# Kernel tuning notes

Hardware: AMD Instinct MI355X
Metric: run time of the kernel (lower is better)

## Reference

```python
import jax, jax.numpy as jnp
import numpy as np

N_S, N_G, E = 4000, 50000, 250000   # sample nodes, gene nodes, edges per relation
D, H, C1, C3 = 128, 4, 32, 64       # input dim, heads, layer-1 per-head dim, layer-3 per-head dim
NEG_SLOPE = 0.2


def gatv2(x_src, x_dst, src, dst, ea, Wl, bl, Wr, br, We, att, bias, n_dst, concat):
    """PyG GATv2Conv (add_self_loops=False, edge_dim=1, eval mode)."""
    Hh, C = att.shape
    xl = (x_src @ Wl + bl).reshape(-1, Hh, C)          # [N_src, H, C]
    xr = (x_dst @ Wr + br).reshape(-1, Hh, C)          # [N_dst, H, C]
    ee = (ea @ We).reshape(-1, Hh, C)                  # [E, H, C]
    m = jax.nn.leaky_relu(xl[src] + xr[dst] + ee, NEG_SLOPE)   # [E, H, C]
    logits = jnp.einsum('ehc,hc->eh', m, att)          # [E, H]
    # segment softmax over incoming edges of each destination node
    lmax = jax.ops.segment_max(logits, dst, num_segments=n_dst)[dst]
    ex = jnp.exp(logits - lmax)
    denom = jax.ops.segment_sum(ex, dst, num_segments=n_dst)[dst]
    alpha = ex / denom                                 # [E, H]
    out = jax.ops.segment_sum(xl[src] * alpha[:, :, None], dst, num_segments=n_dst)  # [N_dst, H, C]
    out = out.reshape(n_dst, Hh * C) if concat else out.mean(axis=1)
    return out + bias


def setup_inputs() -> dict:
    key = jax.random.key(0)
    ks = jax.random.split(key, 40)
    p = lambda i, shape: jax.random.normal(ks[i], shape, dtype=jnp.float32) * 0.05
    HC1, HC3 = H * C1, H * C3
    inp = {
        'x_mrna': p(0, (N_S, D)),
        'x_gene': p(1, (N_G, D)),
        'sg_src': jax.random.randint(ks[2], (E,), 0, N_S),
        'sg_dst': jax.random.randint(ks[3], (E,), 0, N_G),
        'gs_src': jax.random.randint(ks[4], (E,), 0, N_G),
        'gs_dst': jax.random.randint(ks[5], (E,), 0, N_S),
        'ea_sg': p(6, (E, 1)),
        'ea_gs': p(7, (E, 1)),
        # layer-1 GATv2 params, relation mrna->gene
        'Wl1_sg': p(8, (D, HC1)), 'bl1_sg': p(9, (HC1,)),
        'Wr1_sg': p(10, (D, HC1)), 'br1_sg': p(11, (HC1,)),
        'We1_sg': p(12, (1, HC1)), 'att1_sg': p(13, (H, C1)), 'bo1_sg': p(14, (HC1,)),
        # layer-1 GATv2 params, relation gene->mrna
        'Wl1_gs': p(15, (D, HC1)), 'bl1_gs': p(16, (HC1,)),
        'Wr1_gs': p(17, (D, HC1)), 'br1_gs': p(18, (HC1,)),
        'We1_gs': p(19, (1, HC1)), 'att1_gs': p(20, (H, C1)), 'bo1_gs': p(21, (HC1,)),
        # layer-3 GATv2 params, relation gene->mrna (concat=False)
        'Wl3_gs': p(22, (HC1, HC3)), 'bl3_gs': p(23, (HC3,)),
        'Wr3_gs': p(24, (HC1, HC3)), 'br3_gs': p(25, (HC3,)),
        'We3_gs': p(26, (1, HC3)), 'att3_gs': p(27, (H, C3)), 'bo3_gs': p(28, (C3,)),
        # self-loop linears for omic ('mrna') nodes
        'Wsl1': p(29, (D, C1)), 'bsl1': p(30, (C1,)),
        'Wsl3': p(31, (HC1, C3)), 'bsl3': p(32, (C3,)),
    }
    return inp


def reference(x_mrna, x_gene, sg_src, sg_dst, gs_src, gs_dst, ea_sg, ea_gs,
              Wl1_sg, bl1_sg, Wr1_sg, br1_sg, We1_sg, att1_sg, bo1_sg,
              Wl1_gs, bl1_gs, Wr1_gs, br1_gs, We1_gs, att1_gs, bo1_gs,
              Wl3_gs, bl3_gs, Wr3_gs, br3_gs, We3_gs, att3_gs, bo3_gs,
              Wsl1, bsl1, Wsl3, bsl3):
    # ---- layer 1 (HeteroConv over both relations) ----
    x1_gene = gatv2(x_mrna, x_gene, sg_src, sg_dst, ea_sg,
                    Wl1_sg, bl1_sg, Wr1_sg, br1_sg, We1_sg, att1_sg, bo1_sg, N_G, True)
    x1_mrna = gatv2(x_gene, x_mrna, gs_src, gs_dst, ea_gs,
                    Wl1_gs, bl1_gs, Wr1_gs, br1_gs, We1_gs, att1_gs, bo1_gs, N_S, True)
    # self-loop linear on omic nodes, repeated across heads (repeat(1, heads))
    x1_mrna = x1_mrna + jnp.tile(x_mrna @ Wsl1 + bsl1, (1, H))
    x1_mrna = jax.nn.relu(x1_mrna)
    x1_gene = jax.nn.relu(x1_gene)
    # ---- three_layers=False: x2 = x1; layer 3 (concat=False, head mean) ----
    x3_mrna = gatv2(x1_gene, x1_mrna, gs_src, gs_dst, ea_gs,
                    Wl3_gs, bl3_gs, Wr3_gs, br3_gs, We3_gs, att3_gs, bo3_gs, N_S, False)
    x3_mrna = x3_mrna + (x1_mrna @ Wsl3 + bsl3)
    x3_mrna = jax.nn.relu(x3_mrna)
    # integrator=None, single omic view -> squeeze to [N_S, C3]
    return x3_mrna
```

## Files before the change

kernel.cpp:

```cpp
#include <hip/hip_runtime.h>
#include <cstdint>
#include <cstddef>

#define NS 4000
#define NG 50000
#define NE 250000
#define DIM 128
#define NDST_TOT (NG + NS)

typedef __bf16 bf16_t;
typedef bf16_t bf16x8 __attribute__((ext_vector_type(8)));
typedef bf16_t bf16x4 __attribute__((ext_vector_type(4)));
typedef bf16_t bf16x2 __attribute__((ext_vector_type(2)));
typedef float floatx4 __attribute__((ext_vector_type(4)));

#define HIST_B 977
#define WT_TOT 143360
struct HPArgs {
  const int* sgd; const int* gsd;
  int* cnt; unsigned short* rank_sg; unsigned short* rank_gs;
  const float* W[8]; bf16_t* Wt[8]; int N[8]; int e0[8];
  const float* xm; bf16_t* xbm;
  const float* xg; bf16_t* xbg;
};

__global__ __launch_bounds__(256) void histprep(HPArgs a) {
  if (blockIdx.x < HIST_B) {
    int e = blockIdx.x * 256 + threadIdx.x;
    if (e < NE) {
      a.rank_sg[e] = (unsigned short)atomicAdd(a.cnt + a.sgd[e], 1);
      a.rank_gs[e] = (unsigned short)atomicAdd(a.cnt + NG + a.gsd[e], 1);
    }
  } else {
    int u = (blockIdx.x - HIST_B) * 256 + threadIdx.x;
    if (u < WT_TOT) {
      int c = 0;
#pragma unroll
      for (int i = 1; i < 8; i++) if (u >= a.e0[i]) c = i;
      int idx = u - a.e0[c];
      int N = a.N[c];
      int k = idx / N, n = idx - k * N;
      a.Wt[c][n * 128 + k] = (bf16_t)a.W[c][idx];
    } else if (u < WT_TOT + 128000) {
      int j = (u - WT_TOT) * 4;
      float4 v = *reinterpret_cast<const float4*>(a.xm + j);
      bf16x4 b;
      b[0] = (bf16_t)v.x; b[1] = (bf16_t)v.y; b[2] = (bf16_t)v.z; b[3] = (bf16_t)v.w;
      *reinterpret_cast<bf16x4*>(a.xbm + j) = b;
    } else {
      int j = (u - WT_TOT - 128000) * 4;
      float4 v = *reinterpret_cast<const float4*>(a.xg + j);
      bf16x4 b;
      b[0] = (bf16_t)v.x; b[1] = (bf16_t)v.y; b[2] = (bf16_t)v.z; b[3] = (bf16_t)v.w;
      *reinterpret_cast<bf16x4*>(a.xbg + j) = b;
    }
  }
}

__global__ __launch_bounds__(1024) void scan1(const int* __restrict__ cnt,
                                              int* __restrict__ rp,
                                              int* __restrict__ csum, int n) {
  __shared__ int wsum[16];
  int i = blockIdx.x * 1024 + threadIdx.x;
  int lane = threadIdx.x & 63, w = threadIdx.x >> 6;
  int v = (i < n) ? cnt[i] : 0;
  int x = v;
#pragma unroll
  for (int off = 1; off < 64; off <<= 1) {
    int y = __shfl_up(x, off);
    if (lane >= off) x += y;
  }
  if (lane == 63) wsum[w] = x;
  __syncthreads();
  if (w == 0 && lane < 16) {
    int s = wsum[lane];
#pragma unroll
    for (int off = 1; off < 16; off <<= 1) {
      int y = __shfl_up(s, off);
      if (lane >= off) s += y;
    }
    wsum[lane] = s;
  }
  __syncthreads();
  int incl = x + (w ? wsum[w - 1] : 0);
  if (i < n) rp[i] = incl - v;
  if (threadIdx.x == 1023) csum[blockIdx.x] = incl;
}

__global__ __launch_bounds__(1024) void scan3(int* __restrict__ rp,
                                              const int* __restrict__ csum, int n) {
  __shared__ int pfx_s;
  if (threadIdx.x < 64) {
    int lane = threadIdx.x;
    int v = (lane < (int)blockIdx.x) ? csum[lane] : 0;
#pragma unroll
    for (int off = 32; off > 0; off >>= 1) v += __shfl_down(v, off);
    if (lane == 0) pfx_s = v;
  }
  __syncthreads();
  int i = blockIdx.x * 1024 + threadIdx.x;
  if (i < n) rp[i] += pfx_s;
  if (i == 0) rp[n] = 2 * NE;
}

#define SCAT_B 1954
struct SGArgs {
  const int* sgd; const int* gsd; const int* sgs; const int* gss;
  const float* easg; const float* eags;
  const int* rp; const unsigned short* rank_sg; const unsigned short* rank_gs;
  uint2* meta;
  const bf16_t* X[5];
  const bf16_t* Wt[5];
  const float* Bv[5];
  bf16_t* Y[5];
  int M[5];
  int Ncol[5];
  int blk0[5];
};

__global__ __launch_bounds__(256) void scatgemm(SGArgs a) {
  if (blockIdx.x < SCAT_B) {
    int t = blockIdx.x * 256 + threadIdx.x;
    if (t < NE) {
      int d = a.sgd[t];
      uint2 pv; pv.x = (unsigned)a.sgs[t]; pv.y = __float_as_uint(a.easg[t]);
      a.meta[a.rp[d] + a.rank_sg[t]] = pv;
    } else if (t < 2 * NE) {
      int e = t - NE;
      int d = a.gsd[e];
      uint2 pv; pv.x = (unsigned)a.gss[e]; pv.y = __float_as_uint(a.eags[e]);
      a.meta[a.rp[NG + d] + a.rank_gs[e]] = pv;
    }
    return;
  }
  int bid = blockIdx.x - SCAT_B;
  int c = 0;
#pragma unroll
  for (int i = 1; i < 5; i++) if (bid >= a.blk0[i]) c = i;
  const bf16_t* X = a.X[c];
  const bf16_t* Wt = a.Wt[c];
  const float* B = a.Bv[c];
  bf16_t* Y = a.Y[c];
  int M = a.M[c];
  int N = a.Ncol[c];

  int wv = threadIdx.x >> 6, lane = threadIdx.x & 63;
  int m16 = lane & 15, quad = lane >> 4;
  int row0 = (bid - a.blk0[c]) * 64 + wv * 16;
  int arow = row0 + m16;
  const bf16_t* xp = X + (size_t)arow * DIM + quad * 8;

  bf16x8 afrag[4];
#pragma unroll
  for (int kk = 0; kk < 4; kk++) {
    bf16x8 av = {};
    if (arow < M) av = *reinterpret_cast<const bf16x8*>(xp + kk * 32);
    afrag[kk] = av;
  }

  int ncols = N >> 4;
  for (int nt = 0; nt < ncols; nt++) {
    int col = nt * 16 + m16;
    const bf16_t* bptr = Wt + (size_t)col * DIM + quad * 8;
    floatx4 acc = {0.f, 0.f, 0.f, 0.f};
#pragma unroll
    for (int kk = 0; kk < 4; kk++) {
      bf16x8 b = *reinterpret_cast<const bf16x8*>(bptr + kk * 32);
      acc = __builtin_amdgcn_mfma_f32_16x16x32_bf16(afrag[kk], b, acc, 0, 0, 0);
    }
    float bias = B[col];
    int orow = row0 + quad * 4;
#pragma unroll
    for (int r = 0; r < 4; r++)
      if (orow + r < M) Y[(size_t)(orow + r) * N + col] = (bf16_t)(acc[r] + bias);
  }
}

template <int NCFG>
struct GArgs {
  const bf16_t* X[NCFG];
  const bf16_t* Wt[NCFG];
  const float* Bv[NCFG];
  bf16_t* Y[NCFG];
  int M[NCFG];
  int Ncol[NCFG];
  int blk0[NCFG];
};

template <int NCFG>
__global__ __launch_bounds__(256) void gemm_multi(GArgs<NCFG> a) {
  int c = 0;
#pragma unroll
  for (int i = 1; i < NCFG; i++) if ((int)blockIdx.x >= a.blk0[i]) c = i;
  const bf16_t* X = a.X[c];
  const bf16_t* Wt = a.Wt[c];
  const float* B = a.Bv[c];
  bf16_t* Y = a.Y[c];
  int M = a.M[c];
  int N = a.Ncol[c];

  int wv = threadIdx.x >> 6, lane = threadIdx.x & 63;
  int m16 = lane & 15, quad = lane >> 4;
  int row0 = (blockIdx.x - a.blk0[c]) * 64 + wv * 16;
  int arow = row0 + m16;
  const bf16_t* xp = X + (size_t)arow * DIM + quad * 8;

  bf16x8 afrag[4];
#pragma unroll
  for (int kk = 0; kk < 4; kk++) {
    bf16x8 av = {};
    if (arow < M) av = *reinterpret_cast<const bf16x8*>(xp + kk * 32);
    afrag[kk] = av;
  }

  int ncols = N >> 4;
  for (int nt = 0; nt < ncols; nt++) {
    int col = nt * 16 + m16;
    const bf16_t* bptr = Wt + (size_t)col * DIM + quad * 8;
    floatx4 acc = {0.f, 0.f, 0.f, 0.f};
#pragma unroll
    for (int kk = 0; kk < 4; kk++) {
      bf16x8 b = *reinterpret_cast<const bf16x8*>(bptr + kk * 32);
      acc = __builtin_amdgcn_mfma_f32_16x16x32_bf16(afrag[kk], b, acc, 0, 0, 0);
    }
    float bias = B[col];
    int orow = row0 + quad * 4;
#pragma unroll
    for (int r = 0; r < 4; r++)
      if (orow + r < M) Y[(size_t)(orow + r) * N + col] = (bf16_t)(acc[r] + bias);
  }
}

#define SGB 3125
__global__ __launch_bounds__(256) void gatC(
    const int* __restrict__ rp, const uint2* __restrict__ meta,
    const float* __restrict__ WeS, const float* __restrict__ attS,
    const float* __restrict__ boS,
    const bf16_t* __restrict__ xlS, const bf16_t* __restrict__ xrS,
    bf16_t* __restrict__ outS,
    const float* __restrict__ WeG, const float* __restrict__ attG,
    const float* __restrict__ boG,
    const bf16_t* __restrict__ xlG, const bf16_t* __restrict__ xrG,
    const bf16_t* __restrict__ slG, bf16_t* __restrict__ outG) {
  __shared__ uint2 smeta[256];
  __shared__ float lacc[16][128];
  __shared__ float lden[16][4];
  int lane = threadIdx.x & 63, wv = threadIdx.x >> 6;
  int gl = lane & 15, grp = lane >> 4;

  if (blockIdx.x < SGB) {
    int wid = blockIdx.x * 4 + wv;
    int d0 = wid * 4;
    int q = lane < 5 ? lane : 0;
    int rv = rp[d0 + q];
    int beg = __shfl(rv, grp), end = __shfl(rv, grp + 1);
    int dst = d0 + grp;

    float wev[8], atv[8], xrv[8], acc[8];
    *reinterpret_cast<float4*>(wev) = *reinterpret_cast<const float4*>(WeS + gl * 8);
    *reinterpret_cast<float4*>(wev + 4) = *reinterpret_cast<const float4*>(WeS + gl * 8 + 4);
    *reinterpret_cast<float4*>(atv) = *reinterpret_cast<const float4*>(attS + gl * 8);
    *reinterpret_cast<float4*>(atv + 4) = *reinterpret_cast<const float4*>(attS + gl * 8 + 4);
    bf16x8 xrb = *reinterpret_cast<const bf16x8*>(xrS + (size_t)dst * 128 + gl * 8);
#pragma unroll
    for (int v = 0; v < 8; v++) { xrv[v] = (float)xrb[v]; acc[v] = 0.f; }
    float den = 0.f;

    for (int i0 = beg; i0 < end; i0 += 16) {
      int cnt = min(16, end - i0);
      int s_l = 0; float ea_l = 0.f;
      if (gl < cnt) {
        uint2 mv = meta[i0 + gl];
        s_l = (int)mv.x; ea_l = __uint_as_float(mv.y);
      }
      int base = lane & 48;
      float ea = __shfl(ea_l, base);
      bf16x8 xlb = *reinterpret_cast<const bf16x8*>(
          xlS + (size_t)__shfl(s_l, base) * 128 + gl * 8);
      for (int k = 0; k < cnt; k++) {
        bf16x8 cur = xlb;
        float eac = ea;
        if (k + 1 < cnt) {
          ea = __shfl(ea_l, base + k + 1);
          xlb = *reinterpret_cast<const bf16x8*>(
              xlS + (size_t)__shfl(s_l, base + k + 1) * 128 + gl * 8);
        }
        float p = 0.f, xf[8];
#pragma unroll
        for (int v = 0; v < 8; v++) {
          xf[v] = (float)cur[v];
          float z = fmaf(eac, wev[v], xrv[v]) + xf[v];
          z = z > 0.f ? z : 0.2f * z;
          p = fmaf(z, atv[v], p);
        }
        p += __shfl_xor(p, 1);
        p += __shfl_xor(p, 2);
        float ex = __expf(p);
        den += ex;
#pragma unroll
        for (int v = 0; v < 8; v++) acc[v] = fmaf(ex, xf[v], acc[v]);
      }
    }
    float inv = den > 0.f ? 1.f / den : 0.f;
    bf16x8 o;
#pragma unroll
    for (int v = 0; v < 8; v++) {
      float val = acc[v] * inv + boS[gl * 8 + v];
      o[v] = (bf16_t)(val > 0.f ? val : 0.f);
    }
    *reinterpret_cast<bf16x8*>(outS + (size_t)dst * 128 + gl * 8) = o;
  } else {
    int d = (int)blockIdx.x - SGB;
    const int* rpg = rp + NG;
    int G = wv * 4 + grp;
    int tid = threadIdx.x;

    float wev[8], atv[8], xrv[8], acc[8];
    *reinterpret_cast<float4*>(wev) = *reinterpret_cast<const float4*>(WeG + gl * 8);
    *reinterpret_cast<float4*>(wev + 4) = *reinterpret_cast<const float4*>(WeG + gl * 8 + 4);
    *reinterpret_cast<float4*>(atv) = *reinterpret_cast<const float4*>(attG + gl * 8);
    *reinterpret_cast<float4*>(atv + 4) = *reinterpret_cast<const float4*>(attG + gl * 8 + 4);
    bf16x8 xrb = *reinterpret_cast<const bf16x8*>(xrG + (size_t)d * 128 + gl * 8);
#pragma unroll
    for (int v = 0; v < 8; v++) { xrv[v] = (float)xrb[v]; acc[v] = 0.f; }
    float den = 0.f;

    int beg = rpg[d], end = rpg[d + 1];
    for (int base = beg; base < end; base += 256) {
      int cntb = min(256, end - base);
      __syncthreads();
      if (tid < cntb) smeta[tid] = meta[base + tid];
      __syncthreads();
      int e = G;
      uint2 mv; bf16x8 xlb;
      if (e < cntb) {
        mv = smeta[e];
        xlb = *reinterpret_cast<const bf16x8*>(xlG + (size_t)mv.x * 128 + gl * 8);
      }
      while (e < cntb) {
        bf16x8 cur = xlb;
        float eac = __uint_as_float(mv.y);
        int en = e + 16;
        if (en < cntb) {
          mv = smeta[en];
          xlb = *reinterpret_cast<const bf16x8*>(xlG + (size_t)mv.x * 128 + gl * 8);
        }
        float p = 0.f, xf[8];
#pragma unroll
        for (int v = 0; v < 8; v++) {
          xf[v] = (float)cur[v];
          float z = fmaf(eac, wev[v], xrv[v]) + xf[v];
          z = z > 0.f ? z : 0.2f * z;
          p = fmaf(z, atv[v], p);
        }
        p += __shfl_xor(p, 1);
        p += __shfl_xor(p, 2);
        float ex = __expf(p);
        den += ex;
#pragma unroll
        for (int v = 0; v < 8; v++) acc[v] = fmaf(ex, xf[v], acc[v]);
        e = en;
      }
    }
#pragma unroll
    for (int v = 0; v < 8; v++) lacc[G][gl * 8 + v] = acc[v];
    if ((gl & 3) == 0) lden[G][gl >> 2] = den;
    __syncthreads();
    if (wv != 0) return;
    int ch = lane * 2;
    int h = lane >> 4;
    float a0 = 0.f, a1 = 0.f, dh = 0.f;
#pragma unroll
    for (int g2 = 0; g2 < 16; g2++) {
      a0 += lacc[g2][ch];
      a1 += lacc[g2][ch + 1];
      dh += lden[g2][h];
    }
    float inv = dh > 0.f ? 1.f / dh : 0.f;
    float v0 = a0 * inv + boG[ch] + (float)slG[(size_t)d * 32 + (ch & 31)];
    float v1 = a1 * inv + boG[ch + 1] + (float)slG[(size_t)d * 32 + ((ch + 1) & 31)];
    bf16x2 o;
    o[0] = (bf16_t)(v0 > 0.f ? v0 : 0.f);
    o[1] = (bf16_t)(v1 > 0.f ? v1 : 0.f);
    *reinterpret_cast<bf16x2*>(outG + (size_t)d * 128 + ch) = o;
  }
}

__global__ __launch_bounds__(256) void gatE(
    const int* __restrict__ rp, const uint2* __restrict__ meta,
    const float* __restrict__ We, const float* __restrict__ att,
    const bf16_t* __restrict__ xl, const bf16_t* __restrict__ xr,
    const float* __restrict__ bo, const bf16_t* __restrict__ sl,
    float* __restrict__ out) {
  __shared__ uint2 smeta[256];
  __shared__ float lacc[16][256];
  __shared__ float lden[16][4];
  int lane = threadIdx.x & 63, wv = threadIdx.x >> 6;
  int gl = lane & 15, grp = lane >> 4;
  int G = wv * 4 + grp;
  int tid = threadIdx.x;
  int d = blockIdx.x;

  float wev[16], atv[16], xrv[16], acc[16];
#pragma unroll
  for (int b = 0; b < 4; b++) {
    *reinterpret_cast<float4*>(wev + b * 4) =
        *reinterpret_cast<const float4*>(We + gl * 16 + b * 4);
    *reinterpret_cast<float4*>(atv + b * 4) =
        *reinterpret_cast<const float4*>(att + gl * 16 + b * 4);
  }
  {
    bf16x8 r0 = *reinterpret_cast<const bf16x8*>(xr + (size_t)d * 256 + gl * 16);
    bf16x8 r1 = *reinterpret_cast<const bf16x8*>(xr + (size_t)d * 256 + gl * 16 + 8);
#pragma unroll
    for (int v = 0; v < 8; v++) { xrv[v] = (float)r0[v]; xrv[v + 8] = (float)r1[v]; }
  }
#pragma unroll
  for (int v = 0; v < 16; v++) acc[v] = 0.f;
  float den = 0.f;

  int beg = rp[d], end = rp[d + 1];
  for (int base = beg; base < end; base += 256) {
    int cntb = min(256, end - base);
    __syncthreads();
    if (tid < cntb) smeta[tid] = meta[base + tid];
    __syncthreads();
    int e = G;
    uint2 mv; bf16x8 x0, x1;
    if (e < cntb) {
      mv = smeta[e];
      x0 = *reinterpret_cast<const bf16x8*>(xl + (size_t)mv.x * 256 + gl * 16);
      x1 = *reinterpret_cast<const bf16x8*>(xl + (size_t)mv.x * 256 + gl * 16 + 8);
    }
    while (e < cntb) {
      bf16x8 c0 = x0, c1 = x1;
      float eac = __uint_as_float(mv.y);
      int en = e + 16;
      if (en < cntb) {
        mv = smeta[en];
        x0 = *reinterpret_cast<const bf16x8*>(xl + (size_t)mv.x * 256 + gl * 16);
        x1 = *reinterpret_cast<const bf16x8*>(xl + (size_t)mv.x * 256 + gl * 16 + 8);
      }
      float p = 0.f, xf[16];
#pragma unroll
      for (int v = 0; v < 8; v++) { xf[v] = (float)c0[v]; xf[v + 8] = (float)c1[v]; }
#pragma unroll
      for (int v = 0; v < 16; v++) {
        float z = fmaf(eac, wev[v], xrv[v]) + xf[v];
        z = z > 0.f ? z : 0.2f * z;
        p = fmaf(z, atv[v], p);
      }
      p += __shfl_xor(p, 1);
      p += __shfl_xor(p, 2);
      float ex = __expf(p);
      den += ex;
#pragma unroll
      for (int v = 0; v < 16; v++) acc[v] = fmaf(ex, xf[v], acc[v]);
      e = en;
    }
  }
#pragma unroll
  for (int v = 0; v < 16; v++) lacc[G][gl * 16 + v] = acc[v];
  if ((gl & 3) == 0) lden[G][gl >> 2] = den;
  __syncthreads();
  if (wv != 0) return;
  int ch = lane * 4;
  int h = lane >> 4;
  float a[4] = {0.f, 0.f, 0.f, 0.f};
  float dh = 0.f;
#pragma unroll
  for (int g2 = 0; g2 < 16; g2++) {
#pragma unroll
    for (int v = 0; v < 4; v++) a[v] += lacc[g2][ch + v];
    dh += lden[g2][h];
  }
  float inv = dh > 0.f ? 1.f / dh : 0.f;
#pragma unroll
  for (int v = 0; v < 4; v++) {
    float s_ = a[v] * inv;
    s_ += __shfl_xor(s_, 16);
    s_ += __shfl_xor(s_, 32);
    if (lane < 16) {
      int c = (lane & 15) * 4 + v;
      float val = 0.25f * s_ + bo[c] + (float)sl[(size_t)d * 64 + c];
      out[(size_t)d * 64 + c] = val > 0.f ? val : 0.f;
    }
  }
}


static inline int nblk(long long threads) { return (int)((threads + 255) / 256); }
static inline int nrow(int M, int R) { return (M + R - 1) / R; }

extern "C" void kernel_launch(void* const* d_in, const int* in_sizes, int n_in,
                              void* d_out, int out_size, void* d_ws, size_t ws_size,
                              hipStream_t stream) {
  const float* x_mrna = (const float*)d_in[0];
  const float* x_gene = (const float*)d_in[1];
  const int* sg_src = (const int*)d_in[2];
  const int* sg_dst = (const int*)d_in[3];
  const int* gs_src = (const int*)d_in[4];
  const int* gs_dst = (const int*)d_in[5];
  const float* ea_sg = (const float*)d_in[6];
  const float* ea_gs = (const float*)d_in[7];
  const float* Wl1_sg = (const float*)d_in[8];
  const float* bl1_sg = (const float*)d_in[9];
  const float* Wr1_sg = (const float*)d_in[10];
  const float* br1_sg = (const float*)d_in[11];
  const float* We1_sg = (const float*)d_in[12];
  const float* att1_sg = (const float*)d_in[13];
  const float* bo1_sg = (const float*)d_in[14];
  const float* Wl1_gs = (const float*)d_in[15];
  const float* bl1_gs = (const float*)d_in[16];
  const float* Wr1_gs = (const float*)d_in[17];
  const float* br1_gs = (const float*)d_in[18];
  const float* We1_gs = (const float*)d_in[19];
  const float* att1_gs = (const float*)d_in[20];
  const float* bo1_gs = (const float*)d_in[21];
  const float* Wl3_gs = (const float*)d_in[22];
  const float* bl3_gs = (const float*)d_in[23];
  const float* Wr3_gs = (const float*)d_in[24];
  const float* br3_gs = (const float*)d_in[25];
  const float* We3_gs = (const float*)d_in[26];
  const float* att3_gs = (const float*)d_in[27];
  const float* bo3_gs = (const float*)d_in[28];
  const float* Wsl1 = (const float*)d_in[29];
  const float* bsl1 = (const float*)d_in[30];
  const float* Wsl3 = (const float*)d_in[31];
  const float* bsl3 = (const float*)d_in[32];

  float* ws = (float*)d_ws;
  bf16_t* xl1_gs = (bf16_t*)(ws + 0);
  bf16_t* xl1_sg = (bf16_t*)(ws + 3200000);
  bf16_t* xr1_sg = (bf16_t*)(ws + 3456000);
  bf16_t* xr1_gs = (bf16_t*)(ws + 6656000);
  bf16_t* xl3    = (bf16_t*)(ws + 0);
  bf16_t* xr3    = (bf16_t*)(ws + 6400000);
  bf16_t* xb_mrna = (bf16_t*)(ws + 6912000);
  bf16_t* xb_gene = (bf16_t*)(ws + 7168000);
  bf16_t* x1_gene = (bf16_t*)(ws + 10368000);
  bf16_t* x1_mrna = (bf16_t*)(ws + 13568000);
  bf16_t* sl1    = (bf16_t*)(ws + 13824000);
  bf16_t* sl3    = (bf16_t*)(ws + 13856000);
  int*   ib      = (int*)(ws + 13920000);
  int* cnt  = ib + 0;
  int* rpc  = ib + 54000;
  int* csum = ib + 108002;
  unsigned short* rank_sg = (unsigned short*)(ib + 108066);
  unsigned short* rank_gs = (unsigned short*)(ib + 233066);
  uint2* meta = (uint2*)(ib + 358066);
  bf16_t* wtb = (bf16_t*)(ib + 1358066);

  bf16_t* wt_l1sg = wtb + 0;
  bf16_t* wt_r1sg = wtb + 16384;
  bf16_t* wt_l1gs = wtb + 32768;
  bf16_t* wt_r1gs = wtb + 49152;
  bf16_t* wt_l3   = wtb + 65536;
  bf16_t* wt_r3   = wtb + 98304;
  bf16_t* wt_sl1  = wtb + 131072;
  bf16_t* wt_sl3  = wtb + 135168;

  hipMemsetAsync(cnt, 0, 54000 * sizeof(int), stream);

  {
    HPArgs hp;
    hp.sgd = sg_dst; hp.gsd = gs_dst;
    hp.cnt = cnt; hp.rank_sg = rank_sg; hp.rank_gs = rank_gs;
    const float* Wsrc[8] = {Wl1_sg, Wr1_sg, Wl1_gs, Wr1_gs, Wl3_gs, Wr3_gs, Wsl1, Wsl3};
    bf16_t* Wdst[8] = {wt_l1sg, wt_r1sg, wt_l1gs, wt_r1gs, wt_l3, wt_r3, wt_sl1, wt_sl3};
    int Nn[8] = {128, 128, 128, 128, 256, 256, 32, 64};
    int e0[8] = {0, 16384, 32768, 49152, 65536, 98304, 131072, 135168};
    for (int i = 0; i < 8; i++) { hp.W[i] = Wsrc[i]; hp.Wt[i] = Wdst[i]; hp.N[i] = Nn[i]; hp.e0[i] = e0[i]; }
    hp.xm = x_mrna; hp.xbm = xb_mrna;
    hp.xg = x_gene; hp.xbg = xb_gene;
    histprep<<<HIST_B + 7310, 256, 0, stream>>>(hp);
  }

  int nchunks = (NDST_TOT + 1023) / 1024;
  scan1<<<nchunks, 1024, 0, stream>>>(cnt, rpc, csum, NDST_TOT);
  scan3<<<nchunks, 1024, 0, stream>>>(rpc, csum, NDST_TOT);

  {
    SGArgs sa;
    sa.sgd = sg_dst; sa.gsd = gs_dst; sa.sgs = sg_src; sa.gss = gs_src;
    sa.easg = ea_sg; sa.eags = ea_gs;
    sa.rp = rpc; sa.rank_sg = rank_sg; sa.rank_gs = rank_gs; sa.meta = meta;
    const bf16_t* Xs[5] = {xb_mrna, xb_gene, xb_gene, xb_mrna, xb_mrna};
    const bf16_t* Ws[5] = {wt_l1sg, wt_r1sg, wt_l1gs, wt_r1gs, wt_sl1};
    const float* Bs[5] = {bl1_sg, br1_sg, bl1_gs, br1_gs, bsl1};
    bf16_t* Ys[5] = {xl1_sg, xr1_sg, xl1_gs, xr1_gs, sl1};
    int Ms[5] = {NS, NG, NG, NS, NS};
    int Ns[5] = {128, 128, 128, 128, 32};
    int b0 = 0;
    for (int i = 0; i < 5; i++) {
      sa.X[i] = Xs[i]; sa.Wt[i] = Ws[i]; sa.Bv[i] = Bs[i]; sa.Y[i] = Ys[i];
      sa.M[i] = Ms[i]; sa.Ncol[i] = Ns[i]; sa.blk0[i] = b0;
      b0 += nrow(Ms[i], 64);
    }
    scatgemm<<<SCAT_B + b0, 256, 0, stream>>>(sa);
  }

  gatC<<<SGB + NS, 256, 0, stream>>>(
      rpc, meta,
      We1_sg, att1_sg, bo1_sg, xl1_sg, xr1_sg, x1_gene,
      We1_gs, att1_gs, bo1_gs, xl1_gs, xr1_gs, sl1, x1_mrna);

  {
    GArgs<3> ga;
    const bf16_t* Xs[3] = {x1_gene, x1_mrna, x1_mrna};
    const bf16_t* Ws[3] = {wt_l3, wt_r3, wt_sl3};
    const float* Bs[3] = {bl3_gs, br3_gs, bsl3};
    bf16_t* Ys[3] = {xl3, xr3, sl3};
    int Ms[3] = {NG, NS, NS};
    int Ns[3] = {256, 256, 64};
    int b0 = 0;
    for (int i = 0; i < 3; i++) {
      ga.X[i] = Xs[i]; ga.Wt[i] = Ws[i]; ga.Bv[i] = Bs[i]; ga.Y[i] = Ys[i];
      ga.M[i] = Ms[i]; ga.Ncol[i] = Ns[i]; ga.blk0[i] = b0;
      b0 += nrow(Ms[i], 64);
    }
    gemm_multi<3><<<b0, 256, 0, stream>>>(ga);
  }

  gatE<<<NS, 256, 0, stream>>>(rpc + NG, meta, We3_gs, att3_gs,
                               xl3, xr3, bo3_gs, sl3, (float*)d_out);
}
```

Before: 300.4 us.

## Pack edge metadata into 32 bits, fuse scan kernels, interleave scatter with GEMM blocks

Edge metadata (source index plus edge attribute) is packed into one 32-bit word: a 16-bit source index and a bf16 edge attribute. This halves the meta array traffic in the scatter and in all gather/attention kernels. The two-pass scan becomes a single kernel in which each block re-sums all preceding counts, removing one launch. Scatter blocks now handle both relations per thread and are interleaved with GEMM blocks so both kinds of work run together. The trade-offs are reduced precision of the edge attribute and a hard limit of 65536 source nodes.

Measured after the change: 314.8 us. 1.05x slower.

```diff
diff --git a/kernel.cpp b/kernel.cpp
--- a/kernel.cpp
+++ b/kernel.cpp
@@ -13,6 +13,12 @@
 typedef bf16_t bf16x4 __attribute__((ext_vector_type(4)));
 typedef bf16_t bf16x2 __attribute__((ext_vector_type(2)));
 typedef float floatx4 __attribute__((ext_vector_type(4)));
+
+__device__ __forceinline__ unsigned pack_meta(int src, float ea) {
+  union { bf16_t b; unsigned short u; } cv;
+  cv.b = (bf16_t)ea;
+  return (unsigned)src | ((unsigned)cv.u << 16);
+}
 
 #define HIST_B 977
 #define WT_TOT 143360
@@ -57,12 +63,28 @@
   }
 }
 
-__global__ __launch_bounds__(1024) void scan1(const int* __restrict__ cnt,
-                                              int* __restrict__ rp,
-                                              int* __restrict__ csum, int n) {
+__global__ __launch_bounds__(1024) void scan_f(const int* __restrict__ cnt,
+                                               int* __restrict__ rp, int n) {
   __shared__ int wsum[16];
-  int i = blockIdx.x * 1024 + threadIdx.x;
-  int lane = threadIdx.x & 63, w = threadIdx.x >> 6;
+  __shared__ int base_s;
+  int t = threadIdx.x;
+  int lane = t & 63, w = t >> 6;
+  int lim = blockIdx.x * 1024;
+  int s = 0;
+  for (int i = t; i < lim; i += 1024) s += cnt[i];
+#pragma unroll
+  for (int off = 32; off > 0; off >>= 1) s += __shfl_down(s, off);
+  if (lane == 0) wsum[w] = s;
+  __syncthreads();
+  if (t == 0) {
+    int tot = 0;
+#pragma unroll
+    for (int i = 0; i < 16; i++) tot += wsum[i];
+    base_s = tot;
+  }
+  __syncthreads();
+  int base = base_s;
+  int i = blockIdx.x * 1024 + t;
   int v = (i < n) ? cnt[i] : 0;
   int x = v;
 #pragma unroll
@@ -73,42 +95,25 @@
   if (lane == 63) wsum[w] = x;
   __syncthreads();
   if (w == 0 && lane < 16) {
-    int s = wsum[lane];
+    int ss = wsum[lane];
 #pragma unroll
     for (int off = 1; off < 16; off <<= 1) {
-      int y = __shfl_up(s, off);
-      if (lane >= off) s += y;
-    }
-    wsum[lane] = s;
+      int y = __shfl_up(ss, off);
+      if (lane >= off) ss += y;
+    }
+    wsum[lane] = ss;
   }
   __syncthreads();
   int incl = x + (w ? wsum[w - 1] : 0);
-  if (i < n) rp[i] = incl - v;
-  if (threadIdx.x == 1023) csum[blockIdx.x] = incl;
-}
-
-__global__ __launch_bounds__(1024) void scan3(int* __restrict__ rp,
-                                              const int* __restrict__ csum, int n) {
-  __shared__ int pfx_s;
-  if (threadIdx.x < 64) {
-    int lane = threadIdx.x;
-    int v = (lane < (int)blockIdx.x) ? csum[lane] : 0;
-#pragma unroll
-    for (int off = 32; off > 0; off >>= 1) v += __shfl_down(v, off);
-    if (lane == 0) pfx_s = v;
-  }
-  __syncthreads();
-  int i = blockIdx.x * 1024 + threadIdx.x;
-  if (i < n) rp[i] += pfx_s;
+  if (i < n) rp[i] = base + incl - v;
   if (i == 0) rp[n] = 2 * NE;
 }
 
-#define SCAT_B 1954
 struct SGArgs {
   const int* sgd; const int* gsd; const int* sgs; const int* gss;
   const float* easg; const float* eags;
   const int* rp; const unsigned short* rank_sg; const unsigned short* rank_gs;
-  uint2* meta;
+  unsigned* meta;
   const bf16_t* X[5];
   const bf16_t* Wt[5];
   const float* Bv[5];
@@ -119,24 +124,30 @@
 };
 
 __global__ __launch_bounds__(256) void scatgemm(SGArgs a) {
-  if (blockIdx.x < SCAT_B) {
-    int t = blockIdx.x * 256 + threadIdx.x;
-    if (t < NE) {
-      int d = a.sgd[t];
-      uint2 pv; pv.x = (unsigned)a.sgs[t]; pv.y = __float_as_uint(a.easg[t]);
-      a.meta[a.rp[d] + a.rank_sg[t]] = pv;
-    } else if (t < 2 * NE) {
-      int e = t - NE;
-      int d = a.gsd[e];
-      uint2 pv; pv.x = (unsigned)a.gss[e]; pv.y = __float_as_uint(a.eags[e]);
-      a.meta[a.rp[NG + d] + a.rank_gs[e]] = pv;
-    }
-    return;
-  }
-  int bid = blockIdx.x - SCAT_B;
+  int bi = blockIdx.x;
+  int gemm_b;
+  if (bi < 2 * HIST_B) {
+    if ((bi & 1) == 0) {
+      int t = (bi >> 1) * 256 + threadIdx.x;
+      if (t < NE) {
+        int d1 = a.sgd[t];
+        int d2 = a.gsd[t];
+        unsigned p1 = pack_meta(a.sgs[t], a.easg[t]);
+        unsigned p2 = pack_meta(a.gss[t], a.eags[t]);
+        int o1 = a.rp[d1] + a.rank_sg[t];
+        int o2 = a.rp[NG + d2] + a.rank_gs[t];
+        a.meta[o1] = p1;
+        a.meta[o2] = p2;
+      }
+      return;
+    }
+    gemm_b = bi >> 1;
+  } else {
+    gemm_b = HIST_B + (bi - 2 * HIST_B);
+  }
   int c = 0;
 #pragma unroll
-  for (int i = 1; i < 5; i++) if (bid >= a.blk0[i]) c = i;
+  for (int i = 1; i < 5; i++) if (gemm_b >= a.blk0[i]) c = i;
   const bf16_t* X = a.X[c];
   const bf16_t* Wt = a.Wt[c];
   const float* B = a.Bv[c];
@@ -146,7 +157,7 @@
 
   int wv = threadIdx.x >> 6, lane = threadIdx.x & 63;
   int m16 = lane & 15, quad = lane >> 4;
-  int row0 = (bid - a.blk0[c]) * 64 + wv * 16;
+  int row0 = (gemm_b - a.blk0[c]) * 64 + wv * 16;
   int arow = row0 + m16;
   const bf16_t* xp = X + (size_t)arow * DIM + quad * 8;
 
@@ -233,7 +244,7 @@
 
 #define SGB 3125
 __global__ __launch_bounds__(256) void gatC(
-    const int* __restrict__ rp, const uint2* __restrict__ meta,
+    const int* __restrict__ rp, const unsigned* __restrict__ meta,
     const float* __restrict__ WeS, const float* __restrict__ attS,
     const float* __restrict__ boS,
     const bf16_t* __restrict__ xlS, const bf16_t* __restrict__ xrS,
@@ -242,7 +253,7 @@
     const float* __restrict__ boG,
     const bf16_t* __restrict__ xlG, const bf16_t* __restrict__ xrG,
     const bf16_t* __restrict__ slG, bf16_t* __restrict__ outG) {
-  __shared__ uint2 smeta[256];
+  __shared__ unsigned smeta[256];
   __shared__ float lacc[16][128];
   __shared__ float lden[16][4];
   int lane = threadIdx.x & 63, wv = threadIdx.x >> 6;
@@ -268,22 +279,19 @@
 
     for (int i0 = beg; i0 < end; i0 += 16) {
       int cnt = min(16, end - i0);
-      int s_l = 0; float ea_l = 0.f;
-      if (gl < cnt) {
-        uint2 mv = meta[i0 + gl];
-        s_l = (int)mv.x; ea_l = __uint_as_float(mv.y);
-      }
+      int mv_l = 0;
+      if (gl < cnt) mv_l = (int)meta[i0 + gl];
       int base = lane & 48;
-      float ea = __shfl(ea_l, base);
+      int mvk = __shfl(mv_l, base);
       bf16x8 xlb = *reinterpret_cast<const bf16x8*>(
-          xlS + (size_t)__shfl(s_l, base) * 128 + gl * 8);
+          xlS + (size_t)(mvk & 0xFFFF) * 128 + gl * 8);
       for (int k = 0; k < cnt; k++) {
         bf16x8 cur = xlb;
-        float eac = ea;
+        float eac = __uint_as_float((unsigned)mvk & 0xFFFF0000u);
         if (k + 1 < cnt) {
-          ea = __shfl(ea_l, base + k + 1);
+          mvk = __shfl(mv_l, base + k + 1);
           xlb = *reinterpret_cast<const bf16x8*>(
-              xlS + (size_t)__shfl(s_l, base + k + 1) * 128 + gl * 8);
+              xlS + (size_t)(mvk & 0xFFFF) * 128 + gl * 8);
         }
         float p = 0.f, xf[8];
 #pragma unroll
@@ -332,18 +340,18 @@
       if (tid < cntb) smeta[tid] = meta[base + tid];
       __syncthreads();
       int e = G;
-      uint2 mv; bf16x8 xlb;
+      unsigned mv; bf16x8 xlb;
       if (e < cntb) {
         mv = smeta[e];
-        xlb = *reinterpret_cast<const bf16x8*>(xlG + (size_t)mv.x * 128 + gl * 8);
+        xlb = *reinterpret_cast<const bf16x8*>(xlG + (size_t)(mv & 0xFFFF) * 128 + gl * 8);
       }
       while (e < cntb) {
         bf16x8 cur = xlb;
-        float eac = __uint_as_float(mv.y);
+        float eac = __uint_as_float(mv & 0xFFFF0000u);
         int en = e + 16;
         if (en < cntb) {
           mv = smeta[en];
-          xlb = *reinterpret_cast<const bf16x8*>(xlG + (size_t)mv.x * 128 + gl * 8);
+          xlb = *reinterpret_cast<const bf16x8*>(xlG + (size_t)(mv & 0xFFFF) * 128 + gl * 8);
         }
         float p = 0.f, xf[8];
 #pragma unroll
@@ -387,12 +395,12 @@
 }
 
 __global__ __launch_bounds__(256) void gatE(
-    const int* __restrict__ rp, const uint2* __restrict__ meta,
+    const int* __restrict__ rp, const unsigned* __restrict__ meta,
     const float* __restrict__ We, const float* __restrict__ att,
     const bf16_t* __restrict__ xl, const bf16_t* __restrict__ xr,
     const float* __restrict__ bo, const bf16_t* __restrict__ sl,
     float* __restrict__ out) {
-  __shared__ uint2 smeta[256];
+  __shared__ unsigned smeta[256];
   __shared__ float lacc[16][256];
   __shared__ float lden[16][4];
   int lane = threadIdx.x & 63, wv = threadIdx.x >> 6;
@@ -426,20 +434,20 @@
     if (tid < cntb) smeta[tid] = meta[base + tid];
     __syncthreads();
     int e = G;
-    uint2 mv; bf16x8 x0, x1;
+    unsigned mv; bf16x8 x0, x1;
     if (e < cntb) {
       mv = smeta[e];
-      x0 = *reinterpret_cast<const bf16x8*>(xl + (size_t)mv.x * 256 + gl * 16);
-      x1 = *reinterpret_cast<const bf16x8*>(xl + (size_t)mv.x * 256 + gl * 16 + 8);
+      x0 = *reinterpret_cast<const bf16x8*>(xl + (size_t)(mv & 0xFFFF) * 256 + gl * 16);
+      x1 = *reinterpret_cast<const bf16x8*>(xl + (size_t)(mv & 0xFFFF) * 256 + gl * 16 + 8);
     }
     while (e < cntb) {
       bf16x8 c0 = x0, c1 = x1;
-      float eac = __uint_as_float(mv.y);
+      float eac = __uint_as_float(mv & 0xFFFF0000u);
       int en = e + 16;
       if (en < cntb) {
         mv = smeta[en];
-        x0 = *reinterpret_cast<const bf16x8*>(xl + (size_t)mv.x * 256 + gl * 16);
-        x1 = *reinterpret_cast<const bf16x8*>(xl + (size_t)mv.x * 256 + gl * 16 + 8);
+        x0 = *reinterpret_cast<const bf16x8*>(xl + (size_t)(mv & 0xFFFF) * 256 + gl * 16);
+        x1 = *reinterpret_cast<const bf16x8*>(xl + (size_t)(mv & 0xFFFF) * 256 + gl * 16 + 8);
       }
       float p = 0.f, xf[16];
 #pragma unroll
@@ -545,11 +553,10 @@
   int*   ib      = (int*)(ws + 13920000);
   int* cnt  = ib + 0;
   int* rpc  = ib + 54000;
-  int* csum = ib + 108002;
-  unsigned short* rank_sg = (unsigned short*)(ib + 108066);
-  unsigned short* rank_gs = (unsigned short*)(ib + 233066);
-  uint2* meta = (uint2*)(ib + 358066);
-  bf16_t* wtb = (bf16_t*)(ib + 1358066);
+  unsigned short* rank_sg = (unsigned short*)(ib + 108002);
+  unsigned short* rank_gs = (unsigned short*)(ib + 233002);
+  unsigned* meta = (unsigned*)(ib + 358002);
+  bf16_t* wtb = (bf16_t*)(ib + 858002);
 
   bf16_t* wt_l1sg = wtb + 0;
   bf16_t* wt_r1sg = wtb + 16384;
@@ -577,8 +584,7 @@
   }
 
   int nchunks = (NDST_TOT + 1023) / 1024;
-  scan1<<<nchunks, 1024, 0, stream>>>(cnt, rpc, csum, NDST_TOT);
-  scan3<<<nchunks, 1024, 0, stream>>>(rpc, csum, NDST_TOT);
+  scan_f<<<nchunks, 1024, 0, stream>>>(cnt, rpc, NDST_TOT);
 
   {
     SGArgs sa;
@@ -597,7 +603,7 @@
       sa.M[i] = Ms[i]; sa.Ncol[i] = Ns[i]; sa.blk0[i] = b0;
       b0 += nrow(Ms[i], 64);
     }
-    scatgemm<<<SCAT_B + b0, 256, 0, stream>>>(sa);
+    scatgemm<<<HIST_B + b0, 256, 0, stream>>>(sa);
   }
 
   gatC<<<SGB + NS, 256, 0, stream>>>(
```
